# Performance work log

Measured on AMD Instinct MI355X. Metric: run time of the kernel, lower is better.

## Reference

```python
import math
import jax, jax.numpy as jnp
import numpy as np

TOP_K = 2
N_EXP = 8
TRAIN_CAPACITY = 1.25
MIN_CAPACITY = 4


def _capacity(num_tokens):
    cap = math.floor(TOP_K * TRAIN_CAPACITY * num_tokens / N_EXP)
    cap += cap % 2
    return max(cap, MIN_CAPACITY)


def _router(x, w_g):
    B, T, D = x.shape
    N = B * T
    C = _capacity(N)  # static: depends only on shapes

    logits = jnp.einsum('btd,ed->bte', x, w_g)            # [B,T,E]
    _, top_idx = jax.lax.top_k(logits, TOP_K)             # [B,T,K]
    probs = jax.nn.softmax(logits, axis=-1).reshape(N, N_EXP)  # [N,E]
    idx = top_idx.reshape(N, TOP_K)                       # [N,K]

    # one-hot expert mask, laid out [K, N, E] as in the torch code
    exp_mask = jax.nn.one_hot(idx, N_EXP, dtype=jnp.int32)      # [N,K,E]
    exp_mask = jnp.transpose(exp_mask, (1, 0, 2))               # [K,N,E]

    # position of each routed token within its expert's queue
    rank = jnp.cumsum(exp_mask.reshape(TOP_K * N, N_EXP), axis=0)
    rank = rank.reshape(TOP_K, N, N_EXP) - 1                    # [K,N,E]

    exp_mask = exp_mask * (rank < C).astype(jnp.int32)          # drop over-capacity
    used_capacity = jnp.sum(exp_mask, axis=(0, 1))              # [E]
    rank_sel = jnp.sum(exp_mask * rank, axis=-1)                # [K,N] int

    idx_kn = jnp.transpose(idx)                                 # [K,N]
    keep = jnp.take_along_axis(exp_mask, idx_kn[:, :, None], axis=2)[..., 0]  # [K,N]
    p_sel = jnp.transpose(jnp.take_along_axis(probs, idx, axis=1))            # [K,N]
    w = keep.astype(probs.dtype) * p_sel                        # [K,N]

    # cb_weight[n, e, c] = sum_k exp_weights[k,n,e] * one_hot(rank_sel)[k,n,c]
    # implemented as a direct scatter-add instead of materializing the
    # O(K*N*E*C) outer product (dropped tokens contribute weight 0).
    tok = jnp.arange(N)
    cb_weight = jnp.zeros((N, N_EXP, C), probs.dtype)
    cb_weight = cb_weight.at[tok[None, :], idx_kn, rank_sel].add(w)
    sec_mask = cb_weight != 0
    return used_capacity, cb_weight, sec_mask


def setup_inputs() -> dict:
    key = jax.random.key(0)
    kx, kw = jax.random.split(key)
    x = jax.random.normal(kx, (2, 2048, 1024), dtype=jnp.float32)
    w_g = jax.random.normal(kw, (8, 1024), dtype=jnp.float32) * 0.02
    return {"x": x, "w_g": w_g}


def reference(x, w_g):
    return _router(x, w_g)
```

## Files before the change

### kernel.cpp

```cpp
#include <hip/hip_runtime.h>

#define N_TOK 4096
#define DIM   1024
#define NE    8
#define CAP   1280
#define EC    (NE * CAP)
#define EC4   (EC / 4)
#define NEC   ((size_t)N_TOK * EC)

typedef float nt_float4 __attribute__((ext_vector_type(4)));

__global__ __launch_bounds__(256) void k_logits(const float* __restrict__ x,
                                                const float* __restrict__ wg,
                                                int* __restrict__ top_idx,
                                                float* __restrict__ top_p) {
    __shared__ float swg[NE * DIM];
    const float4* wg4 = (const float4*)wg;
    float4* swg4 = (float4*)swg;
#pragma unroll
    for (int i = 0; i < 8; ++i) {
        int t = i * 256 + threadIdx.x;
        swg4[t] = wg4[t];
    }
    __syncthreads();

    const int wave = threadIdx.x >> 6;
    const int lane = threadIdx.x & 63;
    const int token = blockIdx.x * 4 + wave;

    const float4* x4 = (const float4*)(x + (size_t)token * DIM);
    float acc[NE];
#pragma unroll
    for (int e = 0; e < NE; ++e) acc[e] = 0.f;

#pragma unroll
    for (int c = 0; c < 4; ++c) {
        float4 xv = x4[c * 64 + lane];
#pragma unroll
        for (int e = 0; e < NE; ++e) {
            float4 wv = swg4[e * 256 + c * 64 + lane];
            acc[e] += xv.x * wv.x + xv.y * wv.y + xv.z * wv.z + xv.w * wv.w;
        }
    }
#pragma unroll
    for (int e = 0; e < NE; ++e) {
        float v = acc[e];
#pragma unroll
        for (int off = 32; off > 0; off >>= 1)
            v += __shfl_xor(v, off, 64);
        acc[e] = v;
    }

    if (lane == 0) {
        float m = acc[0];
#pragma unroll
        for (int e = 1; e < NE; ++e) m = fmaxf(m, acc[e]);
        float pe[NE];
        float s = 0.f;
#pragma unroll
        for (int e = 0; e < NE; ++e) { pe[e] = expf(acc[e] - m); s += pe[e]; }
        float inv = 1.f / s;

        int i1 = 0; float v1 = acc[0];
#pragma unroll
        for (int e = 1; e < NE; ++e) if (acc[e] > v1) { v1 = acc[e]; i1 = e; }
        int i2 = (i1 == 0) ? 1 : 0; float v2 = acc[i2];
#pragma unroll
        for (int e = 0; e < NE; ++e)
            if (e != i1 && acc[e] > v2) { v2 = acc[e]; i2 = e; }

        top_idx[token]         = i1;
        top_idx[N_TOK + token] = i2;
        top_p[token]           = pe[i1] * inv;
        top_p[N_TOK + token]   = pe[i2] * inv;
    }
}

__global__ __launch_bounds__(256) void k_rank(const int* __restrict__ top_idx,
                                              const float* __restrict__ top_p,
                                              int* __restrict__ slot_tok,
                                              float* __restrict__ slot_w,
                                              float* __restrict__ used) {
    __shared__ int se[2 * N_TOK];
    __shared__ int wsum[4][NE];
    __shared__ int s_start[NE];
    const int t = threadIdx.x;
    const int lane = t & 63;
    const int wave = t >> 6;

    const int4* ti4 = (const int4*)top_idx;
    int4* se4 = (int4*)se;
#pragma unroll
    for (int i = 0; i < 8; ++i)
        se4[i * 256 + t] = ti4[i * 256 + t];
    __syncthreads();

    int cnt[NE];
#pragma unroll
    for (int e = 0; e < NE; ++e) cnt[e] = 0;
    const int base = t * 32;
#pragma unroll
    for (int jj = 0; jj < 32; ++jj) {
        int v = se[base + jj];
#pragma unroll
        for (int e = 0; e < NE; ++e) cnt[e] += (v == e) ? 1 : 0;
    }

    int incl[NE];
#pragma unroll
    for (int e = 0; e < NE; ++e) {
        int s = cnt[e];
#pragma unroll
        for (int off = 1; off < 64; off <<= 1) {
            int u = __shfl_up(s, off, 64);
            if (lane >= off) s += u;
        }
        incl[e] = s;
        if (lane == 63) wsum[wave][e] = s;
    }
    __syncthreads();

    int excl[NE];
#pragma unroll
    for (int e = 0; e < NE; ++e) {
        int off = 0, total = 0;
#pragma unroll
        for (int w = 0; w < 4; ++w) {
            int ws = wsum[w][e];
            off   += (w < wave) ? ws : 0;
            total += ws;
        }
        excl[e] = off + incl[e] - cnt[e];
        if (t == 0) s_start[e] = min(total, CAP);
    }
    if (t < NE) {
        int total = wsum[0][t] + wsum[1][t] + wsum[2][t] + wsum[3][t];
        used[t] = (float)min(total, CAP);
    }

    int run[NE];
#pragma unroll
    for (int e = 0; e < NE; ++e) run[e] = excl[e];
#pragma unroll
    for (int jj = 0; jj < 32; ++jj) {
        int j = base + jj;
        int v = se[j];
        int r = run[0];
#pragma unroll
        for (int e = 1; e < NE; ++e) r = (v == e) ? run[e] : r;
#pragma unroll
        for (int e = 0; e < NE; ++e) run[e] += (v == e) ? 1 : 0;
        if (r < CAP) {
            slot_tok[v * CAP + r] = j & (N_TOK - 1);
            slot_w[v * CAP + r]   = top_p[j];
        }
    }

    __syncthreads();
#pragma unroll
    for (int e = 0; e < NE; ++e) {
        for (int s = s_start[e] + t; s < CAP; s += 256)
            slot_tok[e * CAP + s] = -1;
    }
}

__global__ __launch_bounds__(256) void k_out(const int* __restrict__ slot_tok,
                                             const float* __restrict__ slot_w,
                                             const float* __restrict__ used,
                                             float* __restrict__ out) {
    const int n = blockIdx.x;
    const int t = threadIdx.x;
    if (n == 0 && t < NE) out[t] = used[t];

    nt_float4* cb = (nt_float4*)(out + 8 + (size_t)n * EC);
    nt_float4* mk = (nt_float4*)(out + 8 + NEC + (size_t)n * EC);
    const int4* st4 = (const int4*)slot_tok;
    const float4* sw4 = (const float4*)slot_w;

#pragma unroll
    for (int i = 0; i < EC4 / 256; ++i) {
        int v = t + 256 * i;
        int4 tk = st4[v];
        float4 w = sw4[v];
        nt_float4 c, m;
        c.x = (tk.x == n) ? w.x : 0.f;  m.x = (tk.x == n) ? 1.f : 0.f;
        c.y = (tk.y == n) ? w.y : 0.f;  m.y = (tk.y == n) ? 1.f : 0.f;
        c.z = (tk.z == n) ? w.z : 0.f;  m.z = (tk.z == n) ? 1.f : 0.f;
        c.w = (tk.w == n) ? w.w : 0.f;  m.w = (tk.w == n) ? 1.f : 0.f;
        __builtin_nontemporal_store(c, &cb[v]);
        __builtin_nontemporal_store(m, &mk[v]);
    }
}

extern "C" void kernel_launch(void* const* d_in, const int* in_sizes, int n_in,
                              void* d_out, int out_size, void* d_ws, size_t ws_size,
                              hipStream_t stream) {
    const float* x  = (const float*)d_in[0];
    const float* wg = (const float*)d_in[1];
    float* out = (float*)d_out;
    char* ws = (char*)d_ws;

    int*   top_idx  = (int*)(ws);
    float* top_p    = (float*)(ws + 32768);
    int*   slot_tok = (int*)(ws + 65536);
    float* slot_w   = (float*)(ws + 106496);
    float* used     = (float*)(ws + 147456);

    k_logits<<<N_TOK / 4, 256, 0, stream>>>(x, wg, top_idx, top_p);
    k_rank<<<1, 256, 0, stream>>>(top_idx, top_p, slot_tok, slot_w, used);
    k_out<<<N_TOK, 256, 0, stream>>>(slot_tok, slot_w, used, out);
}
```

Before: 394.3 us.

## Replace slot tables with per-token destination indices in output kernel

The rank kernel now writes, for each routed (k, token) pair, its flat expert*capacity destination index (or -1 if dropped), instead of filling per-slot token and weight tables plus a -1 fill pass. The output kernel reads only two destinations and two weights per token and compares them against each output position, instead of streaming the whole slot table (80 KB) for every one of the 4096 token blocks. This removes repeated global or L2 reads and the tail-fill loop in the single-block rank kernel, in exchange for a few extra integer compares per element. The output write volume of roughly 268 MB is unchanged, so the kernel stays bound by that write.

```diff
diff --git a/kernel.cpp b/kernel.cpp
--- a/kernel.cpp
+++ b/kernel.cpp
@@ -77,13 +77,10 @@
 }
 
 __global__ __launch_bounds__(256) void k_rank(const int* __restrict__ top_idx,
-                                              const float* __restrict__ top_p,
-                                              int* __restrict__ slot_tok,
-                                              float* __restrict__ slot_w,
+                                              int* __restrict__ dest,
                                               float* __restrict__ used) {
     __shared__ int se[2 * N_TOK];
     __shared__ int wsum[4][NE];
-    __shared__ int s_start[NE];
     const int t = threadIdx.x;
     const int lane = t & 63;
     const int wave = t >> 6;
@@ -123,15 +120,11 @@
     int excl[NE];
 #pragma unroll
     for (int e = 0; e < NE; ++e) {
-        int off = 0, total = 0;
-#pragma unroll
-        for (int w = 0; w < 4; ++w) {
-            int ws = wsum[w][e];
-            off   += (w < wave) ? ws : 0;
-            total += ws;
-        }
+        int off = 0;
+#pragma unroll
+        for (int w = 0; w < 4; ++w)
+            off += (w < wave) ? wsum[w][e] : 0;
         excl[e] = off + incl[e] - cnt[e];
-        if (t == 0) s_start[e] = min(total, CAP);
     }
     if (t < NE) {
         int total = wsum[0][t] + wsum[1][t] + wsum[2][t] + wsum[3][t];
@@ -150,43 +143,39 @@
         for (int e = 1; e < NE; ++e) r = (v == e) ? run[e] : r;
 #pragma unroll
         for (int e = 0; e < NE; ++e) run[e] += (v == e) ? 1 : 0;
-        if (r < CAP) {
-            slot_tok[v * CAP + r] = j & (N_TOK - 1);
-            slot_w[v * CAP + r]   = top_p[j];
-        }
-    }
-
-    __syncthreads();
-#pragma unroll
-    for (int e = 0; e < NE; ++e) {
-        for (int s = s_start[e] + t; s < CAP; s += 256)
-            slot_tok[e * CAP + s] = -1;
-    }
-}
-
-__global__ __launch_bounds__(256) void k_out(const int* __restrict__ slot_tok,
-                                             const float* __restrict__ slot_w,
+        dest[j] = (r < CAP) ? (v * CAP + r) : -1;
+    }
+}
+
+__global__ __launch_bounds__(256) void k_out(const int* __restrict__ dest,
+                                             const float* __restrict__ top_p,
                                              const float* __restrict__ used,
                                              float* __restrict__ out) {
     const int n = blockIdx.x;
     const int t = threadIdx.x;
     if (n == 0 && t < NE) out[t] = used[t];
 
+    const int   d0 = dest[n];
+    const int   d1 = dest[N_TOK + n];
+    const float w0 = top_p[n];
+    const float w1 = top_p[N_TOK + n];
+
     nt_float4* cb = (nt_float4*)(out + 8 + (size_t)n * EC);
     nt_float4* mk = (nt_float4*)(out + 8 + NEC + (size_t)n * EC);
-    const int4* st4 = (const int4*)slot_tok;
-    const float4* sw4 = (const float4*)slot_w;
 
 #pragma unroll
     for (int i = 0; i < EC4 / 256; ++i) {
         int v = t + 256 * i;
-        int4 tk = st4[v];
-        float4 w = sw4[v];
+        int b = 4 * v;
         nt_float4 c, m;
-        c.x = (tk.x == n) ? w.x : 0.f;  m.x = (tk.x == n) ? 1.f : 0.f;
-        c.y = (tk.y == n) ? w.y : 0.f;  m.y = (tk.y == n) ? 1.f : 0.f;
-        c.z = (tk.z == n) ? w.z : 0.f;  m.z = (tk.z == n) ? 1.f : 0.f;
-        c.w = (tk.w == n) ? w.w : 0.f;  m.w = (tk.w == n) ? 1.f : 0.f;
+        c.x = (d0 == b)     ? w0 : ((d1 == b)     ? w1 : 0.f);
+        c.y = (d0 == b + 1) ? w0 : ((d1 == b + 1) ? w1 : 0.f);
+        c.z = (d0 == b + 2) ? w0 : ((d1 == b + 2) ? w1 : 0.f);
+        c.w = (d0 == b + 3) ? w0 : ((d1 == b + 3) ? w1 : 0.f);
+        m.x = (d0 == b     || d1 == b)     ? 1.f : 0.f;
+        m.y = (d0 == b + 1 || d1 == b + 1) ? 1.f : 0.f;
+        m.z = (d0 == b + 2 || d1 == b + 2) ? 1.f : 0.f;
+        m.w = (d0 == b + 3 || d1 == b + 3) ? 1.f : 0.f;
         __builtin_nontemporal_store(c, &cb[v]);
         __builtin_nontemporal_store(m, &mk[v]);
     }
@@ -200,13 +189,12 @@
     float* out = (float*)d_out;
     char* ws = (char*)d_ws;
 
-    int*   top_idx  = (int*)(ws);
-    float* top_p    = (float*)(ws + 32768);
-    int*   slot_tok = (int*)(ws + 65536);
-    float* slot_w   = (float*)(ws + 106496);
-    float* used     = (float*)(ws + 147456);
+    int*   top_idx = (int*)(ws);
+    float* top_p   = (float*)(ws + 32768);
+    int*   dest    = (int*)(ws + 65536);
+    float* used    = (float*)(ws + 98304);
 
     k_logits<<<N_TOK / 4, 256, 0, stream>>>(x, wg, top_idx, top_p);
-    k_rank<<<1, 256, 0, stream>>>(top_idx, top_p, slot_tok, slot_w, used);
-    k_out<<<N_TOK, 256, 0, stream>>>(slot_tok, slot_w, used, out);
-}
+    k_rank<<<1, 256, 0, stream>>>(top_idx, dest, used);
+    k_out<<<N_TOK, 256, 0, stream>>>(dest, top_p, used, out);
+}
```

New measurement: 380.4 us. 3.5% less time.
